# Kernel tuning notes

Hardware: AMD Instinct MI355X
Metric: run time of the kernel (lower is better)

Reference implementation:

```python
import jax, jax.numpy as jnp
import numpy as np

TOP_K = 2
NUM_EXPERTS = 8

def setup_inputs() -> dict:
    key = jax.random.key(0)
    k_x, k_r, k_g, k_u, k_d = jax.random.split(key, 5)
    B, L, D, H, E = 1, 2048, 1024, 2048, NUM_EXPERTS
    scale = 0.02  # keep router logits / activations in a sane range
    return {
        "x": jax.random.normal(k_x, (B, L, D), dtype=jnp.float32),
        "router_w": jax.random.normal(k_r, (D, E), dtype=jnp.float32) * scale,
        "gate_w": jax.random.normal(k_g, (E, D, H), dtype=jnp.float32) * scale,
        "up_w": jax.random.normal(k_u, (E, D, H), dtype=jnp.float32) * scale,
        "down_w": jax.random.normal(k_d, (E, H, D), dtype=jnp.float32) * scale,
    }

def reference(x, router_w, gate_w, up_w, down_w):
    # x: (B, L, D)
    B, L, D = x.shape
    T = B * L
    E = router_w.shape[1]
    xf = x.reshape(T, D)

    # --- router: top-k softmax over selected logits (Mixtral-style) ---
    logits = xf @ router_w                      # (T, E)
    top_vals, top_idx = jax.lax.top_k(logits, TOP_K)  # (T, K)
    top_w = jax.nn.softmax(top_vals, axis=-1)   # (T, K)

    # combine weights scattered to dense (T, E); zeros for unrouted experts
    combine = jnp.zeros((T, E), dtype=x.dtype).at[
        jnp.arange(T)[:, None], top_idx
    ].add(top_w)

    # --- experts: SwiGLU, computed per expert, zero-weight tokens masked by combine ---
    gate = jnp.einsum('td,edh->eth', xf, gate_w)   # (E, T, H)
    up = jnp.einsum('td,edh->eth', xf, up_w)       # (E, T, H)
    hidden = jax.nn.silu(gate) * up                # (E, T, H)
    expert_out = jnp.einsum('eth,ehd->etd', hidden, down_w)  # (E, T, D)

    # --- weighted combine (equivalent to scatter_add over sorted assignments) ---
    y = jnp.einsum('etd,te->td', expert_out, combine)  # (T, D)
    return y.reshape(B, L, D)
```

## Files before the change

kernel.cpp:

```cpp
#include <hip/hip_runtime.h>
#include <hip/hip_bf16.h>
#include <stdint.h>

#define T_TOK 2048
#define DIM   1024
#define HDIM  2048
#define NE    8
#define ROWS_PAD 4224
#define TSLOTS 40

typedef __attribute__((ext_vector_type(8))) short bf16x8;
typedef __attribute__((ext_vector_type(8))) unsigned short u16x8;
typedef __attribute__((ext_vector_type(4))) float f32x4;
typedef __attribute__((ext_vector_type(4))) unsigned int u32x4;

__device__ __forceinline__ unsigned short f2bf(float f) {
    union { __hip_bfloat16 h; unsigned short u; } cv;
    cv.h = __float2bfloat16(f);
    return cv.u;
}
__device__ __forceinline__ unsigned int f2bf2(float lo, float hi) {
    union { __hip_bfloat162 h; unsigned int u; } cv;
    cv.h = __float22bfloat162_rn(make_float2(lo, hi));
    return cv.u;
}
__device__ __forceinline__ float bf2f(unsigned short b) {
    union { unsigned int u; float f; } v; v.u = ((unsigned int)b) << 16;
    return v.f;
}

__device__ __forceinline__ void gload16(const void* g, void* l) {
    __builtin_amdgcn_global_load_lds(
        (const __attribute__((address_space(1))) void*)g,
        (__attribute__((address_space(3))) void*)l, 16, 0, 0);
}

__global__ void router_kernel(const float* __restrict__ x, const float* __restrict__ rw,
                              int* __restrict__ counts, int* __restrict__ top_idx,
                              float* __restrict__ top_w) {
    int wid = (blockIdx.x * blockDim.x + threadIdx.x) >> 6;
    int lane = threadIdx.x & 63;
    if (wid >= T_TOK) return;
    float acc[NE];
#pragma unroll
    for (int e = 0; e < NE; ++e) acc[e] = 0.f;
    const float* xr = x + (size_t)wid * DIM;
    for (int i = lane; i < DIM; i += 64) {
        float xv = xr[i];
        const float* wr = rw + (size_t)i * NE;
#pragma unroll
        for (int e = 0; e < NE; ++e) acc[e] += xv * wr[e];
    }
#pragma unroll
    for (int off = 32; off; off >>= 1) {
#pragma unroll
        for (int e = 0; e < NE; ++e) acc[e] += __shfl_xor(acc[e], off, 64);
    }
    if (lane == 0) {
        float v0 = -1e30f, v1 = -1e30f; int i0 = 0, i1 = 0;
#pragma unroll
        for (int e = 0; e < NE; ++e) {
            float v = acc[e];
            if (v > v0) { v1 = v0; i1 = i0; v0 = v; i0 = e; }
            else if (v > v1) { v1 = v; i1 = e; }
        }
        float e1 = __expf(v1 - v0);
        float s = 1.f + e1;
        top_idx[wid * 2]     = i0;
        top_idx[wid * 2 + 1] = i1;
        top_w[wid * 2]     = 1.f / s;
        top_w[wid * 2 + 1] = e1 / s;
        atomicAdd(&counts[i0], 1);
        atomicAdd(&counts[i1], 1);
    }
}

__global__ void scan_kernel(const int* __restrict__ counts, int* __restrict__ offsets,
                            int* __restrict__ cursors,
                            int* __restrict__ tl_e, int* __restrict__ tl_m) {
    if (threadIdx.x == 0) {
        int run = 0;
        for (int e = 0; e < NE; ++e) { offsets[e] = run; cursors[e] = run; run += counts[e]; }
        int n = 0;
        for (int e = 0; e < NE; ++e) {
            int mt = (counts[e] + 127) >> 7;
            for (int m = 0; m < mt && n < 64; ++m) { tl_e[n] = e; tl_m[n] = m; ++n; }
        }
        for (; n < 64; ++n) tl_e[n] = -1;
    }
}

__global__ void gather_kernel(const float* __restrict__ x, const int* __restrict__ top_idx,
                              const float* __restrict__ top_w, int* __restrict__ cursors,
                              int* __restrict__ row_tok, float* __restrict__ row_w,
                              unsigned short* __restrict__ Abuf) {
    int t = blockIdx.x;
    __shared__ int pos[2];
    if (threadIdx.x < 2) {
        int k = threadIdx.x;
        int e = top_idx[t * 2 + k];
        int p = atomicAdd(&cursors[e], 1);
        pos[k] = p;
        row_tok[p] = t;
        row_w[p] = top_w[t * 2 + k];
    }
    __syncthreads();
    const float4* xr = (const float4*)(x + (size_t)t * DIM);
    float4 v = xr[threadIdx.x];
    uint2 b; b.x = f2bf2(v.x, v.y); b.y = f2bf2(v.z, v.w);
    uint2* A4 = (uint2*)Abuf;
    A4[(size_t)pos[0] * (DIM / 4) + threadIdx.x] = b;
    A4[(size_t)pos[1] * (DIM / 4) + threadIdx.x] = b;
}

__global__ __launch_bounds__(256, 3)
void gemm1s_kernel(const unsigned short* __restrict__ Abuf,
                   const float* __restrict__ gw,
                   const float* __restrict__ uw,
                   unsigned short* __restrict__ Hg,
                   unsigned short* __restrict__ Hu,
                   const int* __restrict__ offsets, const int* __restrict__ counts,
                   const int* __restrict__ tl_e, const int* __restrict__ tl_m) {
    const int slot = blockIdx.y;
    const int e = tl_e[slot];
    if (e < 0) return;
    const int mtile = tl_m[slot];
    const int cnt = counts[e];
    const int n0 = blockIdx.x * 64;
    const int row0 = offsets[e] + mtile * 128;
    const float* W = blockIdx.z ? uw : gw;
    unsigned short* Hx = blockIdx.z ? Hu : Hg;

    __shared__ unsigned short AsB[2][128 * 64];
    __shared__ unsigned short Bb[2][64 * 64];

    const int tid = threadIdx.x;
    const int lane = tid & 63;
    const int wave = tid >> 6;
    const int wm = wave >> 1;
    const int wn = wave & 1;

    f32x4 acc[4][2];
#pragma unroll
    for (int i = 0; i < 4; ++i)
#pragma unroll
        for (int j = 0; j < 2; ++j) acc[i][j] = (f32x4){0.f, 0.f, 0.f, 0.f};

    const int srow = tid >> 3;
    const int sc0 = tid & 7;
    const unsigned short* Aab = Abuf + (size_t)row0 * DIM;

    auto stageA = [&](int buf, int kt) {
#pragma unroll
        for (int i = 0; i < 4; ++i) {
            int row = i * 32 + srow;
            int csrc = sc0 ^ (row & 7);
            gload16(Aab + (size_t)row * DIM + kt + csrc * 8,
                    &AsB[buf][(i * 256 + tid) * 8]);
        }
    };

    const int bn = tid & 63;
    const int bc0 = tid >> 6;
    const float* Bgb = W + (size_t)e * DIM * HDIM + n0 + bn;

    float bl[2][8];
    auto bload = [&](int kt) {
#pragma unroll
        for (int cc = 0; cc < 2; ++cc) {
            int c = bc0 + cc * 4;
            const float* gs = Bgb + (size_t)(kt + c * 8) * HDIM;
#pragma unroll
            for (int jj = 0; jj < 8; ++jj)
                bl[cc][jj] = gs[(size_t)jj * HDIM];
        }
    };
    auto bwrite = [&](int buf) {
#pragma unroll
        for (int cc = 0; cc < 2; ++cc) {
            int c = bc0 + cc * 4;
            int la = bn * 64 + ((c ^ (bn & 7)) * 8);
            u32x4 v;
#pragma unroll
            for (int p = 0; p < 4; ++p)
                v[p] = f2bf2(bl[cc][2 * p], bl[cc][2 * p + 1]);
            *(u32x4*)&Bb[buf][la] = v;
        }
    };

    const int rsel = lane & 15;
    const int csrcf = lane >> 4;

    stageA(0, 0);
    bload(0);
    bwrite(0);
    int cur = 0;
    for (int kt = 0; kt < DIM; kt += 64) {
        __syncthreads();
        const bool pre = (kt + 64 < DIM);
        if (pre) { stageA(cur ^ 1, kt + 64); bload(kt + 64); }
        const unsigned short* Ac = AsB[cur];
        const unsigned short* Bc = Bb[cur];
#pragma unroll
        for (int kk = 0; kk < 2; ++kk) {
            bf16x8 af[4], bb[2];
#pragma unroll
            for (int i = 0; i < 4; ++i) {
                int ra = wm * 64 + i * 16 + rsel;
                af[i] = *(const bf16x8*)&Ac[ra * 64 + ((kk * 4 + csrcf) ^ (ra & 7)) * 8];
            }
#pragma unroll
            for (int j = 0; j < 2; ++j) {
                int rb = wn * 32 + j * 16 + rsel;
                bb[j] = *(const bf16x8*)&Bc[rb * 64 + ((kk * 4 + csrcf) ^ (rb & 7)) * 8];
            }
#pragma unroll
            for (int i = 0; i < 4; ++i)
#pragma unroll
                for (int j = 0; j < 2; ++j)
                    acc[i][j] = __builtin_amdgcn_mfma_f32_16x16x32_bf16(af[i], bb[j], acc[i][j], 0, 0, 0);
        }
        if (pre) bwrite(cur ^ 1);
        cur ^= 1;
    }

    const int c = lane & 15, rbase = (lane >> 4) * 4;
    const int obase = offsets[e];
#pragma unroll
    for (int i = 0; i < 4; ++i) {
#pragma unroll
        for (int r = 0; r < 4; ++r) {
            int lrow = mtile * 128 + wm * 64 + i * 16 + rbase + r;
            if (lrow < cnt) {
                size_t orow = (size_t)(obase + lrow);
#pragma unroll
                for (int j = 0; j < 2; ++j)
                    Hx[orow * HDIM + n0 + wn * 32 + j * 16 + c] = f2bf(acc[i][j][r]);
            }
        }
    }
}

__global__ void silu_kernel(const unsigned short* __restrict__ Hg,
                            const unsigned short* __restrict__ Hu,
                            unsigned short* __restrict__ Hbuf) {
    size_t idx = ((size_t)blockIdx.x * 256 + threadIdx.x) * 8;
    u16x8 g8 = *(const u16x8*)&Hg[idx];
    u16x8 u8 = *(const u16x8*)&Hu[idx];
    u16x8 h8;
#pragma unroll
    for (int k = 0; k < 8; ++k) {
        float g = bf2f(g8[k]), u = bf2f(u8[k]);
        h8[k] = f2bf(g * u / (1.f + __expf(-g)));
    }
    *(u16x8*)&Hbuf[idx] = h8;
}

__global__ __launch_bounds__(256, 2)
void gemm2_kernel(const unsigned short* __restrict__ Hbuf,
                  const float* __restrict__ dw,
                  float* __restrict__ y,
                  const int* __restrict__ offsets, const int* __restrict__ counts,
                  const int* __restrict__ row_tok, const float* __restrict__ row_w,
                  const int* __restrict__ tl_e, const int* __restrict__ tl_m) {
    const int slot = blockIdx.y;
    const int e = tl_e[slot];
    if (e < 0) return;
    const int mtile = tl_m[slot];
    const int kc = blockIdx.z;
    const int cnt = counts[e];
    const int n0 = blockIdx.x * 128;
    const int row0 = offsets[e] + mtile * 128;

    __shared__ unsigned short As[2][128 * 64];
    __shared__ unsigned short Bs[2][128 * 64];

    const int tid = threadIdx.x;
    const int lane = tid & 63;
    const int wave = tid >> 6;
    const int wm = wave >> 1, wn = wave & 1;

    f32x4 acc[4][4];
#pragma unroll
    for (int i = 0; i < 4; ++i)
#pragma unroll
        for (int j = 0; j < 4; ++j) acc[i][j] = (f32x4){0.f, 0.f, 0.f, 0.f};

    const int srow0 = tid >> 3;
    const int sc0 = tid & 7;
    const unsigned short* Aab = Hbuf + (size_t)row0 * HDIM;

    auto stageA = [&](int buf, int kt) {
#pragma unroll
        for (int i = 0; i < 4; ++i) {
            int row = i * 32 + srow0;
            int csrc = sc0 ^ (row & 7);
            gload16(Aab + (size_t)row * HDIM + kt + csrc * 8,
                    &As[buf][(i * 256 + tid) * 8]);
        }
    };

    const int bn = tid & 127;
    const int bc0 = (tid >> 7) * 4;
    const float* Bbb = dw + (size_t)e * HDIM * DIM + n0 + bn;

    float bl[4][8];
    auto bload = [&](int kt) {
#pragma unroll
        for (int cc = 0; cc < 4; ++cc) {
            const float* bs = Bbb + (size_t)(kt + (bc0 + cc) * 8) * DIM;
#pragma unroll
            for (int jj = 0; jj < 8; ++jj)
                bl[cc][jj] = bs[(size_t)jj * DIM];
        }
    };
    auto bwrite = [&](int buf) {
#pragma unroll
        for (int cc = 0; cc < 4; ++cc) {
            int c = bc0 + cc;
            int la = bn * 64 + ((c ^ (bn & 7)) * 8);
            u32x4 v;
#pragma unroll
            for (int p = 0; p < 4; ++p)
                v[p] = f2bf2(bl[cc][2 * p], bl[cc][2 * p + 1]);
            *(u32x4*)&Bs[buf][la] = v;
        }
    };

    const int rsel = lane & 15;
    const int csrcf = lane >> 4;

    const int kbeg = kc * (HDIM / 2);
    const int kend = kbeg + (HDIM / 2);

    stageA(0, kbeg);
    bload(kbeg);
    bwrite(0);
    int cur = 0;
    for (int kt = kbeg; kt < kend; kt += 64) {
        __syncthreads();
        const bool pre = (kt + 64 < kend);
        if (pre) { stageA(cur ^ 1, kt + 64); bload(kt + 64); }
        const unsigned short* Ac = As[cur];
        const unsigned short* Bc = Bs[cur];
#pragma unroll
        for (int kk = 0; kk < 2; ++kk) {
            bf16x8 af[4], bf[4];
#pragma unroll
            for (int i = 0; i < 4; ++i) {
                int ra = wm * 64 + i * 16 + rsel;
                af[i] = *(const bf16x8*)&Ac[ra * 64 + ((kk * 4 + csrcf) ^ (ra & 7)) * 8];
                int rb = wn * 64 + i * 16 + rsel;
                bf[i] = *(const bf16x8*)&Bc[rb * 64 + ((kk * 4 + csrcf) ^ (rb & 7)) * 8];
            }
#pragma unroll
            for (int i = 0; i < 4; ++i)
#pragma unroll
                for (int j = 0; j < 4; ++j)
                    acc[i][j] = __builtin_amdgcn_mfma_f32_16x16x32_bf16(af[i], bf[j], acc[i][j], 0, 0, 0);
        }
        if (pre) bwrite(cur ^ 1);
        cur ^= 1;
    }

    const int c = lane & 15, rbase = (lane >> 4) * 4;
    const int obase = offsets[e];
#pragma unroll
    for (int i = 0; i < 4; ++i) {
#pragma unroll
        for (int r = 0; r < 4; ++r) {
            int lrow = mtile * 128 + wm * 64 + i * 16 + rbase + r;
            if (lrow < cnt) {
                int grow = obase + lrow;
                int tok = row_tok[grow];
                float w = row_w[grow];
#pragma unroll
                for (int j = 0; j < 4; ++j) {
                    atomicAdd(&y[(size_t)tok * DIM + n0 + wn * 64 + j * 16 + c], w * acc[i][j][r]);
                }
            }
        }
    }
}

extern "C" void kernel_launch(void* const* d_in, const int* in_sizes, int n_in,
                              void* d_out, int out_size, void* d_ws, size_t ws_size,
                              hipStream_t stream) {
    const float* x  = (const float*)d_in[0];
    const float* rw = (const float*)d_in[1];
    const float* gw = (const float*)d_in[2];
    const float* uw = (const float*)d_in[3];
    const float* dw = (const float*)d_in[4];
    float* y = (float*)d_out;

    char* ws = (char*)d_ws;
    int*   counts  = (int*)(ws + 0);
    int*   cursors = (int*)(ws + 32);
    int*   offsets = (int*)(ws + 64);
    int*   top_idx = (int*)(ws + 128);
    float* top_w   = (float*)(ws + 128 + 16384);
    int*   row_tok = (int*)(ws + 128 + 32768);
    float* row_w   = (float*)(ws + 128 + 32768 + 16896);
    int*   tl_e    = (int*)(ws + 128 + 32768 + 2 * 16896);
    int*   tl_m    = (int*)(ws + 128 + 32768 + 2 * 16896 + 256);
    size_t off = 128 + 32768 + 2 * 16896 + 512;
    off = (off + 255) & ~(size_t)255;
    unsigned short* Abuf = (unsigned short*)(ws + off); off += (size_t)ROWS_PAD * DIM * 2;
    unsigned short* Hbuf = (unsigned short*)(ws + off); off += (size_t)ROWS_PAD * HDIM * 2;
    unsigned short* Hg   = (unsigned short*)(ws + off); off += (size_t)ROWS_PAD * HDIM * 2;
    unsigned short* Hu   = (unsigned short*)(ws + off); off += (size_t)ROWS_PAD * HDIM * 2;
    if (ws_size < off) return;

    hipMemsetAsync(counts, 0, 32, stream);
    hipMemsetAsync(d_out, 0, (size_t)out_size * 4, stream);

    router_kernel<<<T_TOK / 4, 256, 0, stream>>>(x, rw, counts, top_idx, top_w);
    scan_kernel<<<1, 64, 0, stream>>>(counts, offsets, cursors, tl_e, tl_m);
    gather_kernel<<<T_TOK, 256, 0, stream>>>(x, top_idx, top_w, cursors, row_tok, row_w, Abuf);

    gemm1s_kernel<<<dim3(HDIM / 64, TSLOTS, 2), 256, 0, stream>>>(Abuf, gw, uw, Hg, Hu,
                                                                  offsets, counts, tl_e, tl_m);
    silu_kernel<<<(T_TOK * 2 * HDIM) / (256 * 8), 256, 0, stream>>>(Hg, Hu, Hbuf);
    gemm2_kernel<<<dim3(DIM / 128, TSLOTS, 2), 256, 0, stream>>>(Hbuf, dw, y, offsets, counts,
                                                                 row_tok, row_w, tl_e, tl_m);
}
```

Measured before the change: 257.6 us.

## Fuse SiLU into gate GEMM epilogue and gate*up product into down-projection A staging

Removes the standalone SiLU kernel. The gate GEMM now applies SiLU in its epilogue. The down-projection kernel loads both the gate and up activations, multiplies them while staging A into shared memory, and no longer reads a combined hidden buffer. The down-projection tile is shrunk from 128 to 64 columns with occupancy raised to 3 waves per SIMD, which doubles the block count but makes each block read both A buffers through registers instead of async LDS loads. This drops one launch and one full write-then-read of the hidden tensor, at the cost of more A traffic per output column and extra ALU work in gemm2.

Result: faster. 247.7 us (-3.8%).

```diff
diff --git a/kernel.cpp b/kernel.cpp
--- a/kernel.cpp
+++ b/kernel.cpp
@@ -117,7 +117,7 @@
 void gemm1s_kernel(const unsigned short* __restrict__ Abuf,
                    const float* __restrict__ gw,
                    const float* __restrict__ uw,
-                   unsigned short* __restrict__ Hg,
+                   unsigned short* __restrict__ Hs,
                    unsigned short* __restrict__ Hu,
                    const int* __restrict__ offsets, const int* __restrict__ counts,
                    const int* __restrict__ tl_e, const int* __restrict__ tl_m) {
@@ -128,8 +128,9 @@
     const int cnt = counts[e];
     const int n0 = blockIdx.x * 64;
     const int row0 = offsets[e] + mtile * 128;
-    const float* W = blockIdx.z ? uw : gw;
-    unsigned short* Hx = blockIdx.z ? Hu : Hg;
+    const int zu = blockIdx.z;
+    const float* W = zu ? uw : gw;
+    unsigned short* Hx = zu ? Hu : Hs;
 
     __shared__ unsigned short AsB[2][128 * 64];
     __shared__ unsigned short Bb[2][64 * 64];
@@ -234,30 +235,19 @@
             if (lrow < cnt) {
                 size_t orow = (size_t)(obase + lrow);
 #pragma unroll
-                for (int j = 0; j < 2; ++j)
-                    Hx[orow * HDIM + n0 + wn * 32 + j * 16 + c] = f2bf(acc[i][j][r]);
-            }
-        }
-    }
-}
-
-__global__ void silu_kernel(const unsigned short* __restrict__ Hg,
-                            const unsigned short* __restrict__ Hu,
-                            unsigned short* __restrict__ Hbuf) {
-    size_t idx = ((size_t)blockIdx.x * 256 + threadIdx.x) * 8;
-    u16x8 g8 = *(const u16x8*)&Hg[idx];
-    u16x8 u8 = *(const u16x8*)&Hu[idx];
-    u16x8 h8;
-#pragma unroll
-    for (int k = 0; k < 8; ++k) {
-        float g = bf2f(g8[k]), u = bf2f(u8[k]);
-        h8[k] = f2bf(g * u / (1.f + __expf(-g)));
-    }
-    *(u16x8*)&Hbuf[idx] = h8;
-}
-
-__global__ __launch_bounds__(256, 2)
-void gemm2_kernel(const unsigned short* __restrict__ Hbuf,
+                for (int j = 0; j < 2; ++j) {
+                    float v = acc[i][j][r];
+                    if (!zu) v = v / (1.f + __expf(-v));
+                    Hx[orow * HDIM + n0 + wn * 32 + j * 16 + c] = f2bf(v);
+                }
+            }
+        }
+    }
+}
+
+__global__ __launch_bounds__(256, 3)
+void gemm2_kernel(const unsigned short* __restrict__ Hs,
+                  const unsigned short* __restrict__ Hu,
                   const float* __restrict__ dw,
                   float* __restrict__ y,
                   const int* __restrict__ offsets, const int* __restrict__ counts,
@@ -267,48 +257,66 @@
     const int e = tl_e[slot];
     if (e < 0) return;
     const int mtile = tl_m[slot];
-    const int kc = blockIdx.z;
+    const int kc = blockIdx.z & 1;
     const int cnt = counts[e];
-    const int n0 = blockIdx.x * 128;
+    const int n0 = blockIdx.x * 64;
     const int row0 = offsets[e] + mtile * 128;
 
     __shared__ unsigned short As[2][128 * 64];
-    __shared__ unsigned short Bs[2][128 * 64];
+    __shared__ unsigned short Bs[2][64 * 64];
 
     const int tid = threadIdx.x;
     const int lane = tid & 63;
     const int wave = tid >> 6;
     const int wm = wave >> 1, wn = wave & 1;
 
-    f32x4 acc[4][4];
+    f32x4 acc[4][2];
 #pragma unroll
     for (int i = 0; i < 4; ++i)
 #pragma unroll
-        for (int j = 0; j < 4; ++j) acc[i][j] = (f32x4){0.f, 0.f, 0.f, 0.f};
-
-    const int srow0 = tid >> 3;
+        for (int j = 0; j < 2; ++j) acc[i][j] = (f32x4){0.f, 0.f, 0.f, 0.f};
+
+    const int srow = tid >> 3;
     const int sc0 = tid & 7;
-    const unsigned short* Aab = Hbuf + (size_t)row0 * HDIM;
-
-    auto stageA = [&](int buf, int kt) {
+    const unsigned short* Asb = Hs + (size_t)row0 * HDIM;
+    const unsigned short* Aub = Hu + (size_t)row0 * HDIM;
+
+    u16x8 as_[4], au_[4];
+    auto aload = [&](int kt) {
 #pragma unroll
         for (int i = 0; i < 4; ++i) {
-            int row = i * 32 + srow0;
-            int csrc = sc0 ^ (row & 7);
-            gload16(Aab + (size_t)row * HDIM + kt + csrc * 8,
-                    &As[buf][(i * 256 + tid) * 8]);
-        }
-    };
-
-    const int bn = tid & 127;
-    const int bc0 = (tid >> 7) * 4;
+            int row = i * 32 + srow;
+            size_t go = (size_t)row * HDIM + kt + sc0 * 8;
+            as_[i] = *(const u16x8*)&Asb[go];
+            au_[i] = *(const u16x8*)&Aub[go];
+        }
+    };
+    auto awrite = [&](int buf) {
+#pragma unroll
+        for (int i = 0; i < 4; ++i) {
+            int row = i * 32 + srow;
+            int la = row * 64 + ((sc0 ^ (row & 7)) * 8);
+            u32x4 v;
+#pragma unroll
+            for (int p = 0; p < 4; ++p) {
+                float h0 = bf2f(as_[i][2 * p])     * bf2f(au_[i][2 * p]);
+                float h1 = bf2f(as_[i][2 * p + 1]) * bf2f(au_[i][2 * p + 1]);
+                v[p] = f2bf2(h0, h1);
+            }
+            *(u32x4*)&As[buf][la] = v;
+        }
+    };
+
+    const int bn = tid & 63;
+    const int bc0 = tid >> 6;
     const float* Bbb = dw + (size_t)e * HDIM * DIM + n0 + bn;
 
-    float bl[4][8];
+    float bl[2][8];
     auto bload = [&](int kt) {
 #pragma unroll
-        for (int cc = 0; cc < 4; ++cc) {
-            const float* bs = Bbb + (size_t)(kt + (bc0 + cc) * 8) * DIM;
+        for (int cc = 0; cc < 2; ++cc) {
+            int c = bc0 + cc * 4;
+            const float* bs = Bbb + (size_t)(kt + c * 8) * DIM;
 #pragma unroll
             for (int jj = 0; jj < 8; ++jj)
                 bl[cc][jj] = bs[(size_t)jj * DIM];
@@ -316,8 +324,8 @@
     };
     auto bwrite = [&](int buf) {
 #pragma unroll
-        for (int cc = 0; cc < 4; ++cc) {
-            int c = bc0 + cc;
+        for (int cc = 0; cc < 2; ++cc) {
+            int c = bc0 + cc * 4;
             int la = bn * 64 + ((c ^ (bn & 7)) * 8);
             u32x4 v;
 #pragma unroll
@@ -333,33 +341,37 @@
     const int kbeg = kc * (HDIM / 2);
     const int kend = kbeg + (HDIM / 2);
 
-    stageA(0, kbeg);
+    aload(kbeg);
     bload(kbeg);
+    awrite(0);
     bwrite(0);
     int cur = 0;
     for (int kt = kbeg; kt < kend; kt += 64) {
         __syncthreads();
         const bool pre = (kt + 64 < kend);
-        if (pre) { stageA(cur ^ 1, kt + 64); bload(kt + 64); }
+        if (pre) { aload(kt + 64); bload(kt + 64); }
         const unsigned short* Ac = As[cur];
         const unsigned short* Bc = Bs[cur];
 #pragma unroll
         for (int kk = 0; kk < 2; ++kk) {
-            bf16x8 af[4], bf[4];
+            bf16x8 af[4], bf[2];
 #pragma unroll
             for (int i = 0; i < 4; ++i) {
                 int ra = wm * 64 + i * 16 + rsel;
                 af[i] = *(const bf16x8*)&Ac[ra * 64 + ((kk * 4 + csrcf) ^ (ra & 7)) * 8];
-                int rb = wn * 64 + i * 16 + rsel;
-                bf[i] = *(const bf16x8*)&Bc[rb * 64 + ((kk * 4 + csrcf) ^ (rb & 7)) * 8];
+            }
+#pragma unroll
+            for (int j = 0; j < 2; ++j) {
+                int rb = wn * 32 + j * 16 + rsel;
+                bf[j] = *(const bf16x8*)&Bc[rb * 64 + ((kk * 4 + csrcf) ^ (rb & 7)) * 8];
             }
 #pragma unroll
             for (int i = 0; i < 4; ++i)
 #pragma unroll
-                for (int j = 0; j < 4; ++j)
+                for (int j = 0; j < 2; ++j)
                     acc[i][j] = __builtin_amdgcn_mfma_f32_16x16x32_bf16(af[i], bf[j], acc[i][j], 0, 0, 0);
         }
-        if (pre) bwrite(cur ^ 1);
+        if (pre) { awrite(cur ^ 1); bwrite(cur ^ 1); }
         cur ^= 1;
     }
 
@@ -375,8 +387,8 @@
                 int tok = row_tok[grow];
                 float w = row_w[grow];
 #pragma unroll
-                for (int j = 0; j < 4; ++j) {
-                    atomicAdd(&y[(size_t)tok * DIM + n0 + wn * 64 + j * 16 + c], w * acc[i][j][r]);
+                for (int j = 0; j < 2; ++j) {
+                    atomicAdd(&y[(size_t)tok * DIM + n0 + wn * 32 + j * 16 + c], w * acc[i][j][r]);
                 }
             }
         }
@@ -406,8 +418,7 @@
     size_t off = 128 + 32768 + 2 * 16896 + 512;
     off = (off + 255) & ~(size_t)255;
     unsigned short* Abuf = (unsigned short*)(ws + off); off += (size_t)ROWS_PAD * DIM * 2;
-    unsigned short* Hbuf = (unsigned short*)(ws + off); off += (size_t)ROWS_PAD * HDIM * 2;
-    unsigned short* Hg   = (unsigned short*)(ws + off); off += (size_t)ROWS_PAD * HDIM * 2;
+    unsigned short* Hs   = (unsigned short*)(ws + off); off += (size_t)ROWS_PAD * HDIM * 2;
     unsigned short* Hu   = (unsigned short*)(ws + off); off += (size_t)ROWS_PAD * HDIM * 2;
     if (ws_size < off) return;
 
@@ -418,9 +429,8 @@
     scan_kernel<<<1, 64, 0, stream>>>(counts, offsets, cursors, tl_e, tl_m);
     gather_kernel<<<T_TOK, 256, 0, stream>>>(x, top_idx, top_w, cursors, row_tok, row_w, Abuf);
 
-    gemm1s_kernel<<<dim3(HDIM / 64, TSLOTS, 2), 256, 0, stream>>>(Abuf, gw, uw, Hg, Hu,
+    gemm1s_kernel<<<dim3(HDIM / 64, TSLOTS, 2), 256, 0, stream>>>(Abuf, gw, uw, Hs, Hu,
                                                                   offsets, counts, tl_e, tl_m);
-    silu_kernel<<<(T_TOK * 2 * HDIM) / (256 * 8), 256, 0, stream>>>(Hg, Hu, Hbuf);
-    gemm2_kernel<<<dim3(DIM / 128, TSLOTS, 2), 256, 0, stream>>>(Hbuf, dw, y, offsets, counts,
-                                                                 row_tok, row_w, tl_e, tl_m);
-}
+    gemm2_kernel<<<dim3(DIM / 64, TSLOTS, 2), 256, 0, stream>>>(Hs, Hu, dw, y, offsets, counts,
+                                                                row_tok, row_w, tl_e, tl_m);
+}
```
